# Kernel tuning notes

Hardware: AMD Instinct MI355X
Metric: run time of the kernel (lower is better)

## Reference

```python
import jax, jax.numpy as jnp
import numpy as np

B, S, D_MODEL, D_OUT = 4, 4096, 512, 64


def setup_inputs() -> dict:
    key = jax.random.key(0)
    ks = jax.random.split(key, 10)
    query = jax.random.normal(ks[0], (B, S, D_MODEL), dtype=jnp.float32)
    key_t = jax.random.normal(ks[1], (B, S, D_MODEL), dtype=jnp.float32)
    value = jax.random.normal(ks[2], (B, S, D_MODEL), dtype=jnp.float32)
    mask = jax.random.randint(ks[3], (B, S, S), 0, 2, dtype=jnp.int32)
    sc = 1.0 / np.sqrt(D_MODEL)
    Wq = jax.random.uniform(ks[4], (D_MODEL, D_OUT), minval=-sc, maxval=sc, dtype=jnp.float32)
    bq = jnp.zeros((D_OUT,), dtype=jnp.float32)
    Wk = jax.random.uniform(ks[5], (D_MODEL, D_OUT), minval=-sc, maxval=sc, dtype=jnp.float32)
    bk = jnp.zeros((D_OUT,), dtype=jnp.float32)
    Wv = jax.random.uniform(ks[6], (D_MODEL, D_OUT), minval=-sc, maxval=sc, dtype=jnp.float32)
    bv = jnp.zeros((D_OUT,), dtype=jnp.float32)
    return {"query": query, "key": key_t, "value": value, "mask": mask,
            "Wq": Wq, "bq": bq, "Wk": Wk, "bk": bk, "Wv": Wv, "bv": bv}


def reference(query, key, value, mask, Wq, bq, Wk, bk, Wv, bv):
    # Linear projections (single head): [B,S,D_MODEL] @ [D_MODEL,D_OUT] + bias
    q = jnp.einsum('bsd,de->bse', query, Wq) + bq
    k = jnp.einsum('bsd,de->bse', key, Wk) + bk
    v = jnp.einsum('bsd,de->bse', value, Wv) + bv
    dim_k = k.shape[-1]
    scores = jnp.einsum('bqe,bke->bqk', q, k) / jnp.sqrt(jnp.float32(dim_k))  # [B,S,S]
    scores = jnp.where(mask == 0, -jnp.inf, scores)
    weights = jax.nn.softmax(scores, axis=-1)
    # dropout is identity in eval mode / for deterministic reference
    outputs = jnp.einsum('bqk,bke->bqe', weights, v)  # [B,S,D_OUT]
    return outputs
```

## Files before the change

kernel.cpp:

```cpp
#include <hip/hip_runtime.h>
#include <hip/hip_bf16.h>

#define BB 4
#define SS 4096
#define DMODEL 512
#define DOUT 64
#define NKH 4
#define KH (SS / NKH)
#define NIT (KH / 64)

typedef __bf16 bf16_t;
typedef __bf16 bf16x8 __attribute__((ext_vector_type(8)));
typedef float floatx4 __attribute__((ext_vector_type(4)));

__device__ inline void gl_lds16(const void* g, void* l) {
  __builtin_amdgcn_global_load_lds(
      (const __attribute__((address_space(1))) unsigned int*)g,
      (__attribute__((address_space(3))) unsigned int*)l, 16, 0, 0);
}

__global__ __launch_bounds__(256) void wtrans_kernel(
    const float* __restrict__ Wq, const float* __restrict__ Wk,
    const float* __restrict__ Wv, bf16_t* __restrict__ wT) {
  int idx = blockIdx.x * 256 + threadIdx.x;
  int mat = idx >> 12;
  int r   = idx & 4095;
  int e   = r & 63;
  int d0  = (r >> 6) << 3;
  const float* W = (mat == 0) ? Wq : ((mat == 1) ? Wk : Wv);
  bf16_t* dst = wT + (size_t)mat * (DOUT * DMODEL) + (size_t)e * DMODEL + d0;
#pragma unroll
  for (int j = 0; j < 8; ++j) dst[j] = (bf16_t)W[(size_t)(d0 + j) * DOUT + e];
}

__global__ __launch_bounds__(256) void proj_kernel(
    const float* __restrict__ inq, const float* __restrict__ ink,
    const float* __restrict__ inv, const bf16_t* __restrict__ wT,
    const float* __restrict__ bq, const float* __restrict__ bk,
    const float* __restrict__ bv,
    bf16_t* __restrict__ q_ws, bf16_t* __restrict__ k_ws,
    bf16_t* __restrict__ v_wsT) {
  const int mat = blockIdx.x >> 8;
  const int s0  = (blockIdx.x & 255) << 6;
  const int lane = threadIdx.x & 63;
  const int w    = threadIdx.x >> 6;
  const int col  = lane & 15, quad = lane >> 4;

  const float* inp  = (mat == 0) ? inq : ((mat == 1) ? ink : inv);
  const float* bias = (mat == 0) ? bq : ((mat == 1) ? bk : bv);
  const bf16_t* wt  = wT + (size_t)mat * (DOUT * DMODEL);

  const int arow = s0 + w * 16 + col;
  const float* arow_p = inp + (size_t)arow * DMODEL;
  floatx4 acc[4] = {};

  float4 a0 = *(const float4*)(arow_p + quad * 8);
  float4 a1 = *(const float4*)(arow_p + quad * 8 + 4);

  for (int ch = 0; ch < 16; ++ch) {
    const int chn = (ch + 1 < 16) ? ch + 1 : ch;
    float4 n0 = *(const float4*)(arow_p + chn * 32 + quad * 8);
    float4 n1 = *(const float4*)(arow_p + chn * 32 + quad * 8 + 4);

    const int d0 = ch * 32 + quad * 8;
    bf16x8 af;
    af[0] = (bf16_t)a0.x; af[1] = (bf16_t)a0.y; af[2] = (bf16_t)a0.z; af[3] = (bf16_t)a0.w;
    af[4] = (bf16_t)a1.x; af[5] = (bf16_t)a1.y; af[6] = (bf16_t)a1.z; af[7] = (bf16_t)a1.w;
#pragma unroll
    for (int c = 0; c < 4; ++c) {
      bf16x8 bw = *(const bf16x8*)(wt + (size_t)(c * 16 + col) * DMODEL + d0);
      acc[c] = __builtin_amdgcn_mfma_f32_16x16x32_bf16(af, bw, acc[c], 0, 0, 0);
    }
    a0 = n0; a1 = n1;
  }

#pragma unroll
  for (int c = 0; c < 4; ++c) {
    float bcol = bias[c * 16 + col];
#pragma unroll
    for (int r = 0; r < 4; ++r) {
      int row = s0 + w * 16 + quad * 4 + r;
      float v = acc[c][r] + bcol;
      if (mat == 2) {
        int b = row >> 12, sp = row & 4095;
        int kp = sp & 31;
        int slot = ((kp & 12) << 1) | (kp & 3) | ((kp >> 4) << 2);
        int sp2 = (sp & ~31) | slot;
        v_wsT[((size_t)(b * DOUT + c * 16 + col)) * SS + sp2] = (bf16_t)v;
      } else {
        bf16_t* dst = (mat == 0) ? q_ws : k_ws;
        dst[(size_t)row * DOUT + c * 16 + col] = (bf16_t)v;
      }
    }
  }
}

__global__ __launch_bounds__(256, 3) void attn_kernel(
    const bf16_t* __restrict__ q_ws, const bf16_t* __restrict__ k_ws,
    const bf16_t* __restrict__ v_wsT, const int* __restrict__ mask,
    float* __restrict__ O_part, float* __restrict__ l_part) {
  const int bq = blockIdx.x >> 2, kh = blockIdx.x & 3;
  const int b  = bq >> 6;
  const int q0 = (bq & 63) << 6;
  const int kbase = kh * KH;
  const int lane = threadIdx.x & 63;
  const int wi   = threadIdx.x >> 6;
  const int col  = lane & 15, quad = lane >> 4;

  __shared__ __align__(16) bf16_t Kb[2][64 * 64];
  __shared__ __align__(16) bf16_t Vb[2][64 * 64];

  const int qrowA = q0 + wi * 16 + col;
  const bf16_t* qbase = q_ws + ((size_t)(b * SS) + qrowA) * DOUT + quad * 8;
  const bf16x8 qa0 = *(const bf16x8*)(qbase);
  const bf16x8 qa1 = *(const bf16x8*)(qbase + 32);
  const int* mrow = mask + ((size_t)(b * SS) + qrowA) * SS + quad * 4;

  const int srow = lane >> 3;
  const int schk = (lane & 7) ^ srow;

  auto stage = [&](int it, int buf) {
    const int k0 = kbase + it * 64;
#pragma unroll
    for (int j = 0; j < 2; ++j) {
      const int i = wi * 2 + j;
      const int r = i * 8 + srow;
      const char* gK = (const char*)(k_ws + ((size_t)(b * SS) + k0 + r) * DOUT) + schk * 16;
      gl_lds16(gK, (char*)(&Kb[buf][0]) + i * 1024);
      const char* gV = (const char*)(v_wsT + ((size_t)(b * DOUT) + r) * SS + k0) + schk * 16;
      gl_lds16(gV, (char*)(&Vb[buf][0]) + i * 1024);
    }
  };

  int4 mc[4], mn[4];
  auto loadM = [&](int k0, int4 m[4]) {
#pragma unroll
    for (int c = 0; c < 4; ++c)
      m[c] = *(const int4*)(mrow + k0 + c * 16);
  };

  floatx4 o[4] = {};
  float l_acc = 0.f;

  stage(0, 0);
  loadM(kbase, mc);
  __syncthreads();

  for (int it = 0; it < NIT; ++it) {
    const int buf = it & 1;
    const int itn = (it + 1 < NIT) ? it + 1 : it;

    loadM(kbase + itn * 64, mn);
    stage(itn, buf ^ 1);

    floatx4 sacc[4];
#pragma unroll
    for (int c = 0; c < 4; ++c) {
      const int row = c * 16 + col;
      bf16x8 k0f = *(const bf16x8*)((const char*)&Kb[buf][0] + row * 128 + ((quad ^ (col & 7)) * 16));
      bf16x8 k1f = *(const bf16x8*)((const char*)&Kb[buf][0] + row * 128 + (((4 | quad) ^ (col & 7)) * 16));
      floatx4 z = {};
      z = __builtin_amdgcn_mfma_f32_16x16x32_bf16(k0f, qa0, z, 0, 0, 0);
      z = __builtin_amdgcn_mfma_f32_16x16x32_bf16(k1f, qa1, z, 0, 0, 0);
      sacc[c] = z;
    }

    bf16x8 vc[4][2];
#pragma unroll
    for (int c = 0; c < 4; ++c) {
      const int row = c * 16 + col;
      vc[c][0] = *(const bf16x8*)((const char*)&Vb[buf][0] + row * 128 + ((quad ^ (col & 7)) * 16));
      vc[c][1] = *(const bf16x8*)((const char*)&Vb[buf][0] + row * 128 + (((4 | quad) ^ (col & 7)) * 16));
    }

    float lp = 0.f;
    bf16x8 pa0, pa1;
#pragma unroll
    for (int c = 0; c < 4; ++c) {
      const int4 m = mc[c];
      float p0 = (m.x != 0) ? __expf(sacc[c][0] * 0.125f) : 0.f;
      float p1 = (m.y != 0) ? __expf(sacc[c][1] * 0.125f) : 0.f;
      float p2 = (m.z != 0) ? __expf(sacc[c][2] * 0.125f) : 0.f;
      float p3 = (m.w != 0) ? __expf(sacc[c][3] * 0.125f) : 0.f;
      lp += (p0 + p1) + (p2 + p3);
      bf16x8& pa = (c < 2) ? pa0 : pa1;
      const int off = (c & 1) * 4;
      pa[off + 0] = (bf16_t)p0; pa[off + 1] = (bf16_t)p1;
      pa[off + 2] = (bf16_t)p2; pa[off + 3] = (bf16_t)p3;
    }
    lp += __shfl_xor(lp, 16);
    lp += __shfl_xor(lp, 32);
    l_acc += lp;

#pragma unroll
    for (int c = 0; c < 4; ++c) {
      o[c] = __builtin_amdgcn_mfma_f32_16x16x32_bf16(pa0, vc[c][0], o[c], 0, 0, 0);
      o[c] = __builtin_amdgcn_mfma_f32_16x16x32_bf16(pa1, vc[c][1], o[c], 0, 0, 0);
    }

#pragma unroll
    for (int c = 0; c < 4; ++c) mc[c] = mn[c];

    __syncthreads();
  }

  float* Op = O_part + (size_t)blockIdx.x * 64 * 64;
#pragma unroll
  for (int c = 0; c < 4; ++c)
#pragma unroll
    for (int r = 0; r < 4; ++r)
      Op[(wi * 16 + quad * 4 + r) * 64 + c * 16 + col] = o[c][r];
  if (quad == 0) l_part[(size_t)blockIdx.x * 64 + wi * 16 + col] = l_acc;
}

__global__ __launch_bounds__(256) void combine_kernel(
    const float* __restrict__ O_part, const float* __restrict__ l_part,
    float* __restrict__ out) {
  const int idx = blockIdx.x * 256 + threadIdx.x;
  const int base = idx * 4;
  const int row = base >> 6;
  const int c   = base & 63;
  const int t   = row >> 6;
  const int rl  = row & 63;
  float4 s = {0.f, 0.f, 0.f, 0.f};
  float lsum = 0.f;
#pragma unroll
  for (int p = 0; p < NKH; ++p) {
    const float* pp = O_part + (((size_t)(t * NKH + p) * 64 + rl) * 64 + c);
    float4 a = *(const float4*)pp;
    s.x += a.x; s.y += a.y; s.z += a.z; s.w += a.w;
    lsum += l_part[(size_t)(t * NKH + p) * 64 + rl];
  }
  const float inv = 1.0f / lsum;
  float4 r4 = {s.x * inv, s.y * inv, s.z * inv, s.w * inv};
  *(float4*)(out + base) = r4;
}

extern "C" void kernel_launch(void* const* d_in, const int* in_sizes, int n_in,
                              void* d_out, int out_size, void* d_ws, size_t ws_size,
                              hipStream_t stream) {
  const float* query = (const float*)d_in[0];
  const float* key   = (const float*)d_in[1];
  const float* value = (const float*)d_in[2];
  const int*   mask  = (const int*)d_in[3];
  const float* Wq = (const float*)d_in[4];
  const float* bq = (const float*)d_in[5];
  const float* Wk = (const float*)d_in[6];
  const float* bk = (const float*)d_in[7];
  const float* Wv = (const float*)d_in[8];
  const float* bv = (const float*)d_in[9];
  float* out = (float*)d_out;

  bf16_t* q_ws  = (bf16_t*)d_ws;
  bf16_t* k_ws  = q_ws + (size_t)BB * SS * DOUT;
  bf16_t* v_wsT = k_ws + (size_t)BB * SS * DOUT;
  bf16_t* wT    = v_wsT + (size_t)BB * SS * DOUT;
  float*  O_part = (float*)(wT + 3 * DOUT * DMODEL);
  float*  l_part = O_part + (size_t)(BB * 64 * NKH) * 64 * 64;

  hipLaunchKernelGGL(wtrans_kernel, dim3(48), dim3(256), 0, stream, Wq, Wk, Wv, wT);
  hipLaunchKernelGGL(proj_kernel, dim3(768), dim3(256), 0, stream,
                     query, key, value, wT, bq, bk, bv, q_ws, k_ws, v_wsT);
  hipLaunchKernelGGL(attn_kernel, dim3(BB * 64 * NKH), dim3(256), 0, stream,
                     q_ws, k_ws, v_wsT, mask, O_part, l_part);
  hipLaunchKernelGGL(combine_kernel, dim3(1024), dim3(256), 0, stream,
                     O_part, l_part, out);
}
```

Baseline: 476.3 us.

## Double attention query tile to 128 rows per block and prefetch projection weights

The attention kernel now handles 128 query rows per block, two 16-row sub-tiles per wave. Each K/V tile staged in LDS, and the K and V fragments read from it, are reused across both sub-tiles, halving K/V traffic per query row. The cost is more registers per wave (launch bounds lowered to 2 blocks per SM) and half as many blocks, 512, which may underfill the GPU. The projection kernel also software-prefetches weight fragments one chunk ahead to hide global load latency.

```diff
diff --git a/kernel.cpp b/kernel.cpp
--- a/kernel.cpp
+++ b/kernel.cpp
@@ -8,6 +8,7 @@
 #define NKH 4
 #define KH (SS / NKH)
 #define NIT (KH / 64)
+#define QT 128
 
 typedef __bf16 bf16_t;
 typedef __bf16 bf16x8 __attribute__((ext_vector_type(8)));
@@ -54,24 +55,34 @@
   const float* arow_p = inp + (size_t)arow * DMODEL;
   floatx4 acc[4] = {};
 
+  const bf16_t* wrow[4];
+#pragma unroll
+  for (int c = 0; c < 4; ++c) wrow[c] = wt + (size_t)(c * 16 + col) * DMODEL;
+
   float4 a0 = *(const float4*)(arow_p + quad * 8);
   float4 a1 = *(const float4*)(arow_p + quad * 8 + 4);
+  bf16x8 bwc[4], bwn[4];
+#pragma unroll
+  for (int c = 0; c < 4; ++c) bwc[c] = *(const bf16x8*)(wrow[c] + quad * 8);
 
   for (int ch = 0; ch < 16; ++ch) {
     const int chn = (ch + 1 < 16) ? ch + 1 : ch;
-    float4 n0 = *(const float4*)(arow_p + chn * 32 + quad * 8);
-    float4 n1 = *(const float4*)(arow_p + chn * 32 + quad * 8 + 4);
-
-    const int d0 = ch * 32 + quad * 8;
+    const int d0n = chn * 32 + quad * 8;
+    float4 n0 = *(const float4*)(arow_p + d0n);
+    float4 n1 = *(const float4*)(arow_p + d0n + 4);
+#pragma unroll
+    for (int c = 0; c < 4; ++c) bwn[c] = *(const bf16x8*)(wrow[c] + d0n);
+
     bf16x8 af;
     af[0] = (bf16_t)a0.x; af[1] = (bf16_t)a0.y; af[2] = (bf16_t)a0.z; af[3] = (bf16_t)a0.w;
     af[4] = (bf16_t)a1.x; af[5] = (bf16_t)a1.y; af[6] = (bf16_t)a1.z; af[7] = (bf16_t)a1.w;
 #pragma unroll
-    for (int c = 0; c < 4; ++c) {
-      bf16x8 bw = *(const bf16x8*)(wt + (size_t)(c * 16 + col) * DMODEL + d0);
-      acc[c] = __builtin_amdgcn_mfma_f32_16x16x32_bf16(af, bw, acc[c], 0, 0, 0);
-    }
+    for (int c = 0; c < 4; ++c)
+      acc[c] = __builtin_amdgcn_mfma_f32_16x16x32_bf16(af, bwc[c], acc[c], 0, 0, 0);
+
     a0 = n0; a1 = n1;
+#pragma unroll
+    for (int c = 0; c < 4; ++c) bwc[c] = bwn[c];
   }
 
 #pragma unroll
@@ -95,13 +106,13 @@
   }
 }
 
-__global__ __launch_bounds__(256, 3) void attn_kernel(
+__global__ __launch_bounds__(256, 2) void attn_kernel(
     const bf16_t* __restrict__ q_ws, const bf16_t* __restrict__ k_ws,
     const bf16_t* __restrict__ v_wsT, const int* __restrict__ mask,
     float* __restrict__ O_part, float* __restrict__ l_part) {
   const int bq = blockIdx.x >> 2, kh = blockIdx.x & 3;
-  const int b  = bq >> 6;
-  const int q0 = (bq & 63) << 6;
+  const int b  = bq >> 5;
+  const int q0 = (bq & 31) << 7;
   const int kbase = kh * KH;
   const int lane = threadIdx.x & 63;
   const int wi   = threadIdx.x >> 6;
@@ -110,11 +121,16 @@
   __shared__ __align__(16) bf16_t Kb[2][64 * 64];
   __shared__ __align__(16) bf16_t Vb[2][64 * 64];
 
-  const int qrowA = q0 + wi * 16 + col;
-  const bf16_t* qbase = q_ws + ((size_t)(b * SS) + qrowA) * DOUT + quad * 8;
-  const bf16x8 qa0 = *(const bf16x8*)(qbase);
-  const bf16x8 qa1 = *(const bf16x8*)(qbase + 32);
-  const int* mrow = mask + ((size_t)(b * SS) + qrowA) * SS + quad * 4;
+  bf16x8 qa[2][2];
+  const int* mrow[2];
+#pragma unroll
+  for (int s = 0; s < 2; ++s) {
+    const int qrow = q0 + (wi * 2 + s) * 16 + col;
+    const bf16_t* qb = q_ws + ((size_t)(b * SS) + qrow) * DOUT + quad * 8;
+    qa[s][0] = *(const bf16x8*)(qb);
+    qa[s][1] = *(const bf16x8*)(qb + 32);
+    mrow[s] = mask + ((size_t)(b * SS) + qrow) * SS + quad * 4;
+  }
 
   const int srow = lane >> 3;
   const int schk = (lane & 7) ^ srow;
@@ -132,38 +148,51 @@
     }
   };
 
-  int4 mc[4], mn[4];
-  auto loadM = [&](int k0, int4 m[4]) {
-#pragma unroll
-    for (int c = 0; c < 4; ++c)
-      m[c] = *(const int4*)(mrow + k0 + c * 16);
+  int4 mc[2][4], mn[2][4];
+  auto loadM = [&](int k0) {
+#pragma unroll
+    for (int s = 0; s < 2; ++s)
+#pragma unroll
+      for (int c = 0; c < 4; ++c)
+        mn[s][c] = *(const int4*)(mrow[s] + k0 + c * 16);
   };
 
-  floatx4 o[4] = {};
-  float l_acc = 0.f;
+  floatx4 o[2][4] = {};
+  float l_acc[2] = {0.f, 0.f};
 
   stage(0, 0);
-  loadM(kbase, mc);
+  loadM(kbase);
+#pragma unroll
+  for (int s = 0; s < 2; ++s)
+#pragma unroll
+    for (int c = 0; c < 4; ++c) mc[s][c] = mn[s][c];
   __syncthreads();
 
   for (int it = 0; it < NIT; ++it) {
     const int buf = it & 1;
     const int itn = (it + 1 < NIT) ? it + 1 : it;
 
-    loadM(kbase + itn * 64, mn);
+    loadM(kbase + itn * 64);
     stage(itn, buf ^ 1);
 
-    floatx4 sacc[4];
+    bf16x8 kf[4][2];
 #pragma unroll
     for (int c = 0; c < 4; ++c) {
       const int row = c * 16 + col;
-      bf16x8 k0f = *(const bf16x8*)((const char*)&Kb[buf][0] + row * 128 + ((quad ^ (col & 7)) * 16));
-      bf16x8 k1f = *(const bf16x8*)((const char*)&Kb[buf][0] + row * 128 + (((4 | quad) ^ (col & 7)) * 16));
-      floatx4 z = {};
-      z = __builtin_amdgcn_mfma_f32_16x16x32_bf16(k0f, qa0, z, 0, 0, 0);
-      z = __builtin_amdgcn_mfma_f32_16x16x32_bf16(k1f, qa1, z, 0, 0, 0);
-      sacc[c] = z;
-    }
+      kf[c][0] = *(const bf16x8*)((const char*)&Kb[buf][0] + row * 128 + ((quad ^ (col & 7)) * 16));
+      kf[c][1] = *(const bf16x8*)((const char*)&Kb[buf][0] + row * 128 + (((4 | quad) ^ (col & 7)) * 16));
+    }
+
+    floatx4 sacc[2][4];
+#pragma unroll
+    for (int s = 0; s < 2; ++s)
+#pragma unroll
+      for (int c = 0; c < 4; ++c) {
+        floatx4 z = {};
+        z = __builtin_amdgcn_mfma_f32_16x16x32_bf16(kf[c][0], qa[s][0], z, 0, 0, 0);
+        z = __builtin_amdgcn_mfma_f32_16x16x32_bf16(kf[c][1], qa[s][1], z, 0, 0, 0);
+        sacc[s][c] = z;
+      }
 
     bf16x8 vc[4][2];
 #pragma unroll
@@ -173,44 +202,53 @@
       vc[c][1] = *(const bf16x8*)((const char*)&Vb[buf][0] + row * 128 + (((4 | quad) ^ (col & 7)) * 16));
     }
 
-    float lp = 0.f;
-    bf16x8 pa0, pa1;
-#pragma unroll
-    for (int c = 0; c < 4; ++c) {
-      const int4 m = mc[c];
-      float p0 = (m.x != 0) ? __expf(sacc[c][0] * 0.125f) : 0.f;
-      float p1 = (m.y != 0) ? __expf(sacc[c][1] * 0.125f) : 0.f;
-      float p2 = (m.z != 0) ? __expf(sacc[c][2] * 0.125f) : 0.f;
-      float p3 = (m.w != 0) ? __expf(sacc[c][3] * 0.125f) : 0.f;
-      lp += (p0 + p1) + (p2 + p3);
-      bf16x8& pa = (c < 2) ? pa0 : pa1;
-      const int off = (c & 1) * 4;
-      pa[off + 0] = (bf16_t)p0; pa[off + 1] = (bf16_t)p1;
-      pa[off + 2] = (bf16_t)p2; pa[off + 3] = (bf16_t)p3;
-    }
-    lp += __shfl_xor(lp, 16);
-    lp += __shfl_xor(lp, 32);
-    l_acc += lp;
-
-#pragma unroll
-    for (int c = 0; c < 4; ++c) {
-      o[c] = __builtin_amdgcn_mfma_f32_16x16x32_bf16(pa0, vc[c][0], o[c], 0, 0, 0);
-      o[c] = __builtin_amdgcn_mfma_f32_16x16x32_bf16(pa1, vc[c][1], o[c], 0, 0, 0);
-    }
-
-#pragma unroll
-    for (int c = 0; c < 4; ++c) mc[c] = mn[c];
+#pragma unroll
+    for (int s = 0; s < 2; ++s) {
+      float lp = 0.f;
+      bf16x8 pa0, pa1;
+#pragma unroll
+      for (int c = 0; c < 4; ++c) {
+        const int4 m = mc[s][c];
+        float p0 = (m.x != 0) ? __expf(sacc[s][c][0] * 0.125f) : 0.f;
+        float p1 = (m.y != 0) ? __expf(sacc[s][c][1] * 0.125f) : 0.f;
+        float p2 = (m.z != 0) ? __expf(sacc[s][c][2] * 0.125f) : 0.f;
+        float p3 = (m.w != 0) ? __expf(sacc[s][c][3] * 0.125f) : 0.f;
+        lp += (p0 + p1) + (p2 + p3);
+        bf16x8& pa = (c < 2) ? pa0 : pa1;
+        const int off = (c & 1) * 4;
+        pa[off + 0] = (bf16_t)p0; pa[off + 1] = (bf16_t)p1;
+        pa[off + 2] = (bf16_t)p2; pa[off + 3] = (bf16_t)p3;
+      }
+      lp += __shfl_xor(lp, 16);
+      lp += __shfl_xor(lp, 32);
+      l_acc[s] += lp;
+
+#pragma unroll
+      for (int c = 0; c < 4; ++c) {
+        o[s][c] = __builtin_amdgcn_mfma_f32_16x16x32_bf16(pa0, vc[c][0], o[s][c], 0, 0, 0);
+        o[s][c] = __builtin_amdgcn_mfma_f32_16x16x32_bf16(pa1, vc[c][1], o[s][c], 0, 0, 0);
+      }
+    }
+
+#pragma unroll
+    for (int s = 0; s < 2; ++s)
+#pragma unroll
+      for (int c = 0; c < 4; ++c) mc[s][c] = mn[s][c];
 
     __syncthreads();
   }
 
-  float* Op = O_part + (size_t)blockIdx.x * 64 * 64;
-#pragma unroll
-  for (int c = 0; c < 4; ++c)
-#pragma unroll
-    for (int r = 0; r < 4; ++r)
-      Op[(wi * 16 + quad * 4 + r) * 64 + c * 16 + col] = o[c][r];
-  if (quad == 0) l_part[(size_t)blockIdx.x * 64 + wi * 16 + col] = l_acc;
+  float* Op = O_part + (size_t)blockIdx.x * (QT * 64);
+#pragma unroll
+  for (int s = 0; s < 2; ++s) {
+#pragma unroll
+    for (int c = 0; c < 4; ++c)
+#pragma unroll
+      for (int r = 0; r < 4; ++r)
+        Op[((wi * 2 + s) * 16 + quad * 4 + r) * 64 + c * 16 + col] = o[s][c][r];
+    if (quad == 0)
+      l_part[(size_t)blockIdx.x * QT + (wi * 2 + s) * 16 + col] = l_acc[s];
+  }
 }
 
 __global__ __launch_bounds__(256) void combine_kernel(
@@ -220,16 +258,16 @@
   const int base = idx * 4;
   const int row = base >> 6;
   const int c   = base & 63;
-  const int t   = row >> 6;
-  const int rl  = row & 63;
+  const int t   = row >> 7;
+  const int rl  = row & 127;
   float4 s = {0.f, 0.f, 0.f, 0.f};
   float lsum = 0.f;
 #pragma unroll
   for (int p = 0; p < NKH; ++p) {
-    const float* pp = O_part + (((size_t)(t * NKH + p) * 64 + rl) * 64 + c);
+    const float* pp = O_part + (((size_t)(t * NKH + p) * QT + rl) * 64 + c);
     float4 a = *(const float4*)pp;
     s.x += a.x; s.y += a.y; s.z += a.z; s.w += a.w;
-    lsum += l_part[(size_t)(t * NKH + p) * 64 + rl];
+    lsum += l_part[(size_t)(t * NKH + p) * QT + rl];
   }
   const float inv = 1.0f / lsum;
   float4 r4 = {s.x * inv, s.y * inv, s.z * inv, s.w * inv};
@@ -256,12 +294,13 @@
   bf16_t* v_wsT = k_ws + (size_t)BB * SS * DOUT;
   bf16_t* wT    = v_wsT + (size_t)BB * SS * DOUT;
   float*  O_part = (float*)(wT + 3 * DOUT * DMODEL);
-  float*  l_part = O_part + (size_t)(BB * 64 * NKH) * 64 * 64;
-
+  float*  l_part = O_part + (size_t)(BB * (SS / QT) * NKH) * QT * 64;
+
+  const int attn_grid = BB * (SS / QT) * NKH;
   hipLaunchKernelGGL(wtrans_kernel, dim3(48), dim3(256), 0, stream, Wq, Wk, Wv, wT);
   hipLaunchKernelGGL(proj_kernel, dim3(768), dim3(256), 0, stream,
                      query, key, value, wT, bq, bk, bv, q_ws, k_ws, v_wsT);
-  hipLaunchKernelGGL(attn_kernel, dim3(BB * 64 * NKH), dim3(256), 0, stream,
+  hipLaunchKernelGGL(attn_kernel, dim3(attn_grid), dim3(256), 0, stream,
                      q_ws, k_ws, v_wsT, mask, O_part, l_part);
   hipLaunchKernelGGL(combine_kernel, dim3(1024), dim3(256), 0, stream,
                      O_part, l_part, out);
```

Result: no change. 475.3 us (-0.2%).
